# Optimization experiments

Measured on AMD Instinct MI355X. Metric: run time of the kernel, lower is better.

## Reference

```python
import jax, jax.numpy as jnp
import numpy as np

V, E, H, D = 32000, 512, 512, 512  # vocab, emb_dim, enc_hid_dim, dec_hid_dim
B, S, T = 32, 64, 48               # batch, src_len, trg_len


def _gru_cell(x, h, Wih, Whh, bih, bhh):
    # PyTorch GRU cell semantics (gate order r, z, n)
    gi = x @ Wih.T + bih
    gh = h @ Whh.T + bhh
    ir, iz, i_n = jnp.split(gi, 3, axis=-1)
    hr, hz, h_n = jnp.split(gh, 3, axis=-1)
    r = jax.nn.sigmoid(ir + hr)
    z = jax.nn.sigmoid(iz + hz)
    n = jnp.tanh(i_n + r * h_n)
    return (1.0 - z) * n + z * h


def setup_inputs() -> dict:
    key = jax.random.key(0)
    ks = jax.random.split(key, 21)
    f = lambda k, shp: jax.random.normal(k, shp, dtype=jnp.float32) * 0.05
    inp = {
        'src': jax.random.randint(ks[0], (B, S), 0, V),
        'trg': jax.random.randint(ks[1], (T, B), 0, V),
        'emb': f(ks[2], (V, E)),
        'encf_Wih': f(ks[3], (3 * H, E)), 'encf_Whh': f(ks[4], (3 * H, H)),
        'encf_bih': f(ks[5], (3 * H,)), 'encf_bhh': f(ks[6], (3 * H,)),
        'encb_Wih': f(ks[7], (3 * H, E)), 'encb_Whh': f(ks[8], (3 * H, H)),
        'encb_bih': f(ks[9], (3 * H,)), 'encb_bhh': f(ks[10], (3 * H,)),
        'fc_W': f(ks[11], (D, 2 * H)), 'fc_b': f(ks[12], (D,)),
        'attn_W': f(ks[13], (D, D + 2 * H)), 'attn_v': f(ks[14], (D,)),
        'dec_Wih': f(ks[15], (3 * D, E + 2 * H)), 'dec_Whh': f(ks[16], (3 * D, D)),
        'dec_bih': f(ks[17], (3 * D,)), 'dec_bhh': f(ks[18], (3 * D,)),
        'out_W': f(ks[19], (V, 2 * H + D + E)),
        'out_b': jnp.zeros((V,), dtype=jnp.float32),
    }
    return inp


def _forward(src, trg, emb, encf_Wih, encf_Whh, encf_bih, encf_bhh,
             encb_Wih, encb_Whh, encb_bih, encb_bhh, fc_W, fc_b,
             attn_W, attn_v, dec_Wih, dec_Whh, dec_bih, dec_bhh, out_W, out_b):
    x = emb[src]                       # [B,S,E]
    xT = jnp.swapaxes(x, 0, 1)         # [S,B,E]
    h0 = jnp.zeros((src.shape[0], encf_Whh.shape[1]), dtype=x.dtype)

    def stepf(h, xt):
        h2 = _gru_cell(xt, h, encf_Wih, encf_Whh, encf_bih, encf_bhh)
        return h2, h2

    def stepb(h, xt):
        h2 = _gru_cell(xt, h, encb_Wih, encb_Whh, encb_bih, encb_bhh)
        return h2, h2

    hf, yf = jax.lax.scan(stepf, h0, xT)
    hb, yb = jax.lax.scan(stepb, h0, xT[::-1])
    # [B,S,2H] bidirectional encoder outputs (backward stream re-reversed)
    enc_out = jnp.concatenate([jnp.swapaxes(yf, 0, 1), jnp.swapaxes(yb[::-1], 0, 1)], axis=-1)
    # decoder init state from final fwd/bwd hidden
    s0 = jnp.tanh(jnp.concatenate([hf, hb], axis=-1) @ fc_W.T + fc_b)  # [B,D]

    def dec_step(s, tok):
        e = emb[tok]  # [B,E]
        srep = jnp.broadcast_to(s[:, None, :], (s.shape[0], enc_out.shape[1], s.shape[1]))
        energy = jnp.tanh(jnp.concatenate([srep, enc_out], axis=-1) @ attn_W.T)  # [B,S,D]
        a = jax.nn.softmax(energy @ attn_v, axis=1)  # [B,S]
        c = jnp.einsum('bs,bsh->bh', a, enc_out)     # [B,2H]
        s2 = _gru_cell(jnp.concatenate([e, c], axis=-1), s, dec_Wih, dec_Whh, dec_bih, dec_bhh)
        pred = jnp.concatenate([s2, c, e], axis=-1) @ out_W.T + out_b  # [B,V]
        return s2, pred

    # teacher forcing: decoder inputs are trg[0..T-2]
    _, preds = jax.lax.scan(dec_step, s0, trg[:-1])
    out0 = jnp.zeros((1,) + preds.shape[1:], dtype=preds.dtype)  # outputs[0] stays zero
    return jnp.concatenate([out0, preds], axis=0)  # [T,B,V]


def reference(src, trg, emb, encf_Wih, encf_Whh, encf_bih, encf_bhh,
              encb_Wih, encb_Whh, encb_bih, encb_bhh, fc_W, fc_b,
              attn_W, attn_v, dec_Wih, dec_Whh, dec_bih, dec_bhh, out_W, out_b):
    return _forward(src, trg, emb, encf_Wih, encf_Whh, encf_bih, encf_bhh,
                    encb_Wih, encb_Whh, encb_bih, encb_bhh, fc_W, fc_b,
                    attn_W, attn_v, dec_Wih, dec_Whh, dec_bih, dec_bhh, out_W, out_b)
```

## Files before the change

kernel.cpp:

```cpp
#include <hip/hip_runtime.h>
#include <stdint.h>
#include <stddef.h>

typedef __attribute__((ext_vector_type(8))) short short8;
typedef __attribute__((ext_vector_type(4))) float f32x4;
typedef unsigned int u32;

__device__ inline unsigned short f2bf(float f) {
  union { float f; uint32_t u; } v; v.f = f;
  uint32_t u = v.u;
  u += 0x7FFFu + ((u >> 16) & 1u);
  return (unsigned short)(u >> 16);
}
__device__ inline float bf2f(unsigned short h) {
  union { uint32_t u; float f; } v; v.u = ((uint32_t)h) << 16; return v.f;
}
__device__ inline float bflo(u32 v) {
  union { u32 u; float f; } x; x.u = v << 16; return x.f;
}
__device__ inline float bfhi(u32 v) {
  union { u32 u; float f; } x; x.u = v & 0xffff0000u; return x.f;
}
__device__ inline short8 pack8(float4 a, float4 b) {
  short8 r;
  r[0] = (short)f2bf(a.x); r[1] = (short)f2bf(a.y);
  r[2] = (short)f2bf(a.z); r[3] = (short)f2bf(a.w);
  r[4] = (short)f2bf(b.x); r[5] = (short)f2bf(b.y);
  r[6] = (short)f2bf(b.z); r[7] = (short)f2bf(b.w);
  return r;
}
__device__ inline float tanh_fast(float x) {
  float xc = fminf(fmaxf(x, -9.f), 9.f);
  float e = __expf(2.f * xc);
  return (e - 1.f) * __builtin_amdgcn_rcpf(e + 1.f);
}
__device__ inline float sigm_fast(float x) {
  float xc = fminf(fmaxf(x, -30.f), 30.f);
  return __builtin_amdgcn_rcpf(1.f + __expf(-xc));
}
__device__ inline void gl_lds16(const unsigned short* g, unsigned short* l) {
  __builtin_amdgcn_global_load_lds(
      (const __attribute__((address_space(1))) u32*)g,
      (__attribute__((address_space(3))) u32*)l, 16, 0, 0);
}

__global__ __launch_bounds__(128) void prep_gather(
    const int* __restrict__ src, const int* __restrict__ trg,
    const float* __restrict__ emb,
    unsigned short* __restrict__ xbf, unsigned short* __restrict__ ebf,
    unsigned short* __restrict__ Zbf,
    float* __restrict__ outZero,
    unsigned short* __restrict__ hbf,
    float* __restrict__ hf32,
    const float* __restrict__ encfW, const float* __restrict__ encbW,
    const float* __restrict__ attnW, const float* __restrict__ decWhh,
    unsigned short* __restrict__ whFbf, unsigned short* __restrict__ whBbf,
    unsigned short* __restrict__ Wcat) {
  int r = blockIdx.x, tid = threadIdx.x;
  if (r >= 3624) {
    if (tid >= 64) return;
    int q = r - 3624;
    int c = tid * 8;
    const float* s;
    unsigned short* d;
    if (q < 1536) { s = encfW + (size_t)q * 512 + c; d = whFbf + (size_t)q * 512 + c; }
    else if (q < 3072) { int u = q - 1536; s = encbW + (size_t)u * 512 + c; d = whBbf + (size_t)u * 512 + c; }
    else if (q < 3584) { int u = q - 3072; s = attnW + (size_t)u * 1536 + c; d = Wcat + (size_t)u * 512 + c; }
    else { int u = q - 3584; s = decWhh + (size_t)u * 512 + c; d = Wcat + (size_t)(u + 512) * 512 + c; }
    *(short8*)d = pack8(*(const float4*)s, *(const float4*)(s + 4));
    return;
  }
  if (r >= 3584) {
    int z = r - 3584;
    if (z < 32) {
      float4* dst = (float4*)(outZero + (size_t)z * 32000);
      for (int i = tid; i < 8000; i += 128) dst[i] = (float4){0.f, 0.f, 0.f, 0.f};
    } else if (z < 36) {
      float4* dst = (float4*)(hbf + (size_t)(z - 32) * 32768);
      for (int i = tid; i < 4096; i += 128) dst[i] = (float4){0.f, 0.f, 0.f, 0.f};
    } else if (z < 40) {
      float4* dst = (float4*)(hf32 + (size_t)(z - 36) * 32768);
      for (int i = tid; i < 8192; i += 128) dst[i] = (float4){0.f, 0.f, 0.f, 0.f};
    }
    return;
  }
  if (r < 2048) {
    int b = r & 31, s = r >> 5;
    int tok = src[b * 64 + s];
    const float* e = emb + (size_t)tok * 512;
    float4 v = *(const float4*)(e + tid * 4);
    unsigned short* dst = xbf + (size_t)r * 512 + tid * 4;
    dst[0] = f2bf(v.x); dst[1] = f2bf(v.y); dst[2] = f2bf(v.z); dst[3] = f2bf(v.w);
  } else {
    int rr = r - 2048;
    int t = rr >> 5, b = rr & 31;
    unsigned short* dst = ebf + (size_t)rr * 512 + tid * 4;
    if (t < 47) {
      int tok = trg[t * 32 + b];
      const float* e = emb + (size_t)tok * 512;
      float4 v = *(const float4*)(e + tid * 4);
      unsigned short q0 = f2bf(v.x), q1 = f2bf(v.y), q2 = f2bf(v.z), q3 = f2bf(v.w);
      dst[0] = q0; dst[1] = q1; dst[2] = q2; dst[3] = q3;
      unsigned short* zd = Zbf + (size_t)rr * 2048 + 1536 + tid * 4;
      zd[0] = q0; zd[1] = q1; zd[2] = q2; zd[3] = q3;
    } else {
      dst[0] = 0; dst[1] = 0; dst[2] = 0; dst[3] = 0;
    }
  }
}

template <bool ABF, bool BBF, bool WBF>
__device__ inline void gemm_body(
    const void* __restrict__ Av, int lda,
    const void* __restrict__ Bv, int ldb, int bco,
    const float* __restrict__ bias,
    void* __restrict__ Cv, int ldc,
    int K, int Mvalid, int row_off, int m0, int n0) {
  __shared__ __align__(16) unsigned short As[128 * 32];
  __shared__ __align__(16) unsigned short Bs[128 * 32];
  const int tid = threadIdx.x;
  const int w = tid >> 6, lane = tid & 63;
  const int wm = w >> 1, wn = w & 1;
  const int fr = lane & 15, fq = lane >> 4;
  f32x4 acc[4][4];
#pragma unroll
  for (int mi = 0; mi < 4; ++mi)
#pragma unroll
    for (int ni = 0; ni < 4; ++ni) acc[mi][ni] = (f32x4){0.f, 0.f, 0.f, 0.f};
  for (int k0 = 0; k0 < K; k0 += 32) {
#pragma unroll
    for (int p = 0; p < 2; ++p) {
      int idx = p * 256 + tid;
      int row = idx >> 2, seg = idx & 3;
      if (ABF) {
        const unsigned short* Ab = (const unsigned short*)Av;
        *(short8*)(As + row * 32 + seg * 8) =
            *(const short8*)(Ab + (size_t)(m0 + row) * lda + k0 + seg * 8);
      } else {
        const float* Af = (const float*)Av;
        const float* ap = Af + (size_t)(m0 + row) * lda + k0 + seg * 8;
        *(short8*)(As + row * 32 + seg * 8) = pack8(*(const float4*)ap, *(const float4*)(ap + 4));
      }
      if (BBF) {
        const unsigned short* Bb = (const unsigned short*)Bv;
        *(short8*)(Bs + row * 32 + seg * 8) =
            *(const short8*)(Bb + (size_t)(n0 + row) * ldb + bco + k0 + seg * 8);
      } else {
        const float* Bf = (const float*)Bv;
        const float* bp = Bf + (size_t)(n0 + row) * ldb + bco + k0 + seg * 8;
        *(short8*)(Bs + row * 32 + seg * 8) = pack8(*(const float4*)bp, *(const float4*)(bp + 4));
      }
    }
    __syncthreads();
    short8 af[4], bfr[4];
#pragma unroll
    for (int mi = 0; mi < 4; ++mi)
      af[mi] = *(const short8*)(As + (wm * 64 + mi * 16 + fr) * 32 + fq * 8);
#pragma unroll
    for (int ni = 0; ni < 4; ++ni)
      bfr[ni] = *(const short8*)(Bs + (wn * 64 + ni * 16 + fr) * 32 + fq * 8);
#pragma unroll
    for (int mi = 0; mi < 4; ++mi)
#pragma unroll
      for (int ni = 0; ni < 4; ++ni)
        acc[mi][ni] = __builtin_amdgcn_mfma_f32_16x16x32_bf16(af[mi], bfr[ni], acc[mi][ni], 0, 0, 0);
    __syncthreads();
  }
#pragma unroll
  for (int mi = 0; mi < 4; ++mi)
#pragma unroll
    for (int ni = 0; ni < 4; ++ni) {
      int col = n0 + wn * 64 + ni * 16 + fr;
      float bv = bias ? bias[col] : 0.f;
#pragma unroll
      for (int j = 0; j < 4; ++j) {
        int rowm = m0 + wm * 64 + mi * 16 + fq * 4 + j;
        if (rowm < Mvalid) {
          float val = acc[mi][ni][j] + bv;
          if (WBF)
            ((unsigned short*)Cv)[(size_t)(rowm + row_off) * ldc + col] = f2bf(val);
          else
            ((float*)Cv)[(size_t)(rowm + row_off) * ldc + col] = val;
        }
      }
    }
}

template <bool ABF, bool BBF, bool WBF>
__global__ __launch_bounds__(256) void gemm_kernel(
    const void* __restrict__ Av, int lda,
    const void* __restrict__ Bv, int ldb, int bco,
    const float* __restrict__ bias,
    void* __restrict__ Cv, int ldc,
    int K, int Mvalid, int row_off) {
  gemm_body<ABF, BBF, WBF>(Av, lda, Bv, ldb, bco, bias, Cv, ldc, K, Mvalid,
                           row_off, blockIdx.x * 128, blockIdx.y * 128);
}

__global__ __launch_bounds__(256) void gemm_fc(
    const float* __restrict__ hcat, const float* __restrict__ fcW,
    const float* __restrict__ fcb,
    float* __restrict__ sf32, unsigned short* __restrict__ sbf) {
  __shared__ __align__(16) unsigned short As[128 * 32];
  __shared__ __align__(16) unsigned short Bs[128 * 32];
  const int tid = threadIdx.x;
  const int n0 = blockIdx.x * 128;
  const int w = tid >> 6, lane = tid & 63;
  const int wm = w >> 1, wn = w & 1;
  const int fr = lane & 15, fq = lane >> 4;
  f32x4 acc[4][4];
#pragma unroll
  for (int mi = 0; mi < 4; ++mi)
#pragma unroll
    for (int ni = 0; ni < 4; ++ni) acc[mi][ni] = (f32x4){0.f, 0.f, 0.f, 0.f};
  for (int k0 = 0; k0 < 1024; k0 += 32) {
#pragma unroll
    for (int p = 0; p < 2; ++p) {
      int idx = p * 256 + tid;
      int row = idx >> 2, seg = idx & 3;
      if (row < 32) {
        const float* ap = hcat + (size_t)row * 1024 + k0 + seg * 8;
        *(short8*)(As + row * 32 + seg * 8) = pack8(*(const float4*)ap, *(const float4*)(ap + 4));
      }
      const float* bp = fcW + (size_t)(n0 + row) * 1024 + k0 + seg * 8;
      *(short8*)(Bs + row * 32 + seg * 8) = pack8(*(const float4*)bp, *(const float4*)(bp + 4));
    }
    __syncthreads();
    short8 af, bfr[4];
    af = *(const short8*)(As + ((wm == 0 ? fr : fr + 16)) * 32 + fq * 8);
#pragma unroll
    for (int ni = 0; ni < 4; ++ni)
      bfr[ni] = *(const short8*)(Bs + (wn * 64 + ni * 16 + fr) * 32 + fq * 8);
#pragma unroll
    for (int ni = 0; ni < 4; ++ni)
      acc[0][ni] = __builtin_amdgcn_mfma_f32_16x16x32_bf16(af, bfr[ni], acc[0][ni], 0, 0, 0);
    __syncthreads();
  }
#pragma unroll
  for (int ni = 0; ni < 4; ++ni) {
    int col = n0 + wn * 64 + ni * 16 + fr;
    float bv = fcb[col];
#pragma unroll
    for (int j = 0; j < 4; ++j) {
      int rowm = (wm == 0 ? 0 : 16) + fq * 4 + j;
      float val = tanhf(acc[0][ni][j] + bv);
      sf32[(size_t)rowm * 512 + col] = val;
      sbf[(size_t)rowm * 512 + col] = f2bf(val);
    }
  }
}

__global__ __launch_bounds__(256) void gemm_gi(
    const unsigned short* __restrict__ xbf, const unsigned short* __restrict__ ebf,
    const float* __restrict__ encfW, const float* __restrict__ encbW,
    const float* __restrict__ decWih,
    const float* __restrict__ bihF, const float* __restrict__ bihB,
    const float* __restrict__ bihD,
    float* __restrict__ Gif, float* __restrict__ Gib, float* __restrict__ Gie) {
  const int z = blockIdx.z;
  const unsigned short* A;
  const float* B;
  const float* bias;
  float* C;
  int ldb, Mvalid;
  if (z == 0) { A = xbf; B = encfW; ldb = 512; bias = bihF; C = Gif; Mvalid = 2048; }
  else if (z == 1) { A = xbf; B = encbW; ldb = 512; bias = bihB; C = Gib; Mvalid = 2048; }
  else {
    if (blockIdx.x >= 12) return;
    A = ebf; B = decWih; ldb = 1536; bias = bihD; C = Gie; Mvalid = 1536;
  }
  gemm_body<true, false, false>(A, 512, B, ldb, 0, bias, C, 1536, 512, Mvalid, 0,
                                blockIdx.x * 128, blockIdx.y * 128);
}

__global__ __launch_bounds__(256) void gemm_ep(
    const unsigned short* __restrict__ ebo,
    const float* __restrict__ attnW, const float* __restrict__ decWih,
    unsigned short* __restrict__ epf, unsigned short* __restrict__ EP2b) {
  const int z = blockIdx.z;
  if (z == 0 && blockIdx.y >= 4) return;
  if (z == 0)
    gemm_body<true, false, true>(ebo, 1024, attnW, 1536, 512, nullptr, epf, 512,
                                 1024, 2048, 0, blockIdx.x * 128, blockIdx.y * 128);
  else
    gemm_body<true, false, true>(ebo, 1024, decWih, 1536, 512, nullptr, EP2b, 1536,
                                 1024, 2048, 0, blockIdx.x * 128, blockIdx.y * 128);
}

__global__ __launch_bounds__(512, 1) void gemm_big8(
    const unsigned short* __restrict__ A,
    const unsigned short* __restrict__ B,
    const float* __restrict__ bias,
    float* __restrict__ C) {
  extern __shared__ char lds[];
  char* LA = lds;
  char* LB = lds + 65536;
  const int tid = threadIdx.x;
  const int w = tid >> 6, lane = tid & 63;
  int wg = blockIdx.x;
  {
    int x = wg & 7, i = wg >> 3;
    wg = (x < 6 ? x * 94 : 564 + (x - 6) * 93) + i;
  }
  const int m0 = (wg % 6) * 256, n0 = (wg / 6) * 256;
  const int wm = w >> 2, wn = w & 3;
  const int fr = lane & 15, fq = lane >> 4;

  auto stage = [&](const unsigned short* G, char* L, int rowbase, int kt, int h, int c) {
#pragma unroll
    for (int j = 0; j < 2; ++j) {
      int pbh = j * 8192 + w * 1024;
      int pl = pbh + lane * 16;
      int lb = pl ^ (((pl >> 7) & 7) << 4);
      int rl = lb >> 7, ch = (lb >> 4) & 7;
      gl_lds16(G + (size_t)(rowbase + h * 128 + rl) * 2048 + kt * 64 + ch * 8,
               (unsigned short*)(L + c * 32768 + h * 16384 + pbh));
    }
  };

  f32x4 acc[8][4];
#pragma unroll
  for (int mi = 0; mi < 8; ++mi)
#pragma unroll
    for (int ni = 0; ni < 4; ++ni) acc[mi][ni] = (f32x4){0.f, 0.f, 0.f, 0.f};

  stage(A, LA, m0, 0, 0, 0); stage(B, LB, n0, 0, 0, 0);
  stage(A, LA, m0, 0, 1, 0); stage(B, LB, n0, 0, 1, 0);
  asm volatile("s_waitcnt vmcnt(0)" ::: "memory");
  __builtin_amdgcn_s_barrier();

  short8 bfrag[8];
  for (int kt = 0; kt < 32; ++kt) {
    const int c = kt & 1;
    char* Abuf = LA + c * 32768;
    char* Bbuf = LB + c * 32768;
#pragma unroll
    for (int p = 0; p < 4; ++p) {
      if (kt < 31) {
        if (p == 0) {
          stage(A, LA, m0, kt + 1, 0, c ^ 1);
          stage(B, LB, n0, kt + 1, 0, c ^ 1);
        } else if (p == 1) {
          stage(A, LA, m0, kt + 1, 1, c ^ 1);
          stage(B, LB, n0, kt + 1, 1, c ^ 1);
        }
      }
      if (p == 0) {
#pragma unroll
        for (int ni = 0; ni < 4; ++ni)
#pragma unroll
          for (int ks = 0; ks < 2; ++ks) {
            int n = wn * 64 + ni * 16 + fr;
            int h = n >> 7, nl = n & 127;
            int lb = nl * 128 + ks * 64 + fq * 16;
            int pb = lb ^ (((lb >> 7) & 7) << 4);
            bfrag[ni * 2 + ks] = *(const short8*)(Bbuf + h * 16384 + pb);
          }
      }
      short8 afrag[4];
#pragma unroll
      for (int q = 0; q < 2; ++q)
#pragma unroll
        for (int ks = 0; ks < 2; ++ks) {
          int r = wm * 128 + (2 * p + q) * 16 + fr;
          int h = r >> 7, rl = r & 127;
          int lb = rl * 128 + ks * 64 + fq * 16;
          int pb = lb ^ (((lb >> 7) & 7) << 4);
          afrag[q * 2 + ks] = *(const short8*)(Abuf + h * 16384 + pb);
        }
      __builtin_amdgcn_s_setprio(1);
#pragma unroll
      for (int q = 0; q < 2; ++q)
#pragma unroll
        for (int ni = 0; ni < 4; ++ni)
#pragma unroll
          for (int ks = 0; ks < 2; ++ks)
            acc[2 * p + q][ni] = __builtin_amdgcn_mfma_f32_16x16x32_bf16(
                afrag[q * 2 + ks], bfrag[ni * 2 + ks], acc[2 * p + q][ni], 0, 0, 0);
      __builtin_amdgcn_s_setprio(0);
      if (p == 3) asm volatile("s_waitcnt vmcnt(0)" ::: "memory");
      __builtin_amdgcn_s_barrier();
    }
  }
#pragma unroll
  for (int mi = 0; mi < 8; ++mi)
#pragma unroll
    for (int ni = 0; ni < 4; ++ni) {
      int col = n0 + wn * 64 + ni * 16 + fr;
      float bv = bias[col];
#pragma unroll
      for (int j = 0; j < 4; ++j) {
        int row = m0 + wm * 128 + mi * 16 + fq * 4 + j;
        if (row < 1504) C[(size_t)(row + 32) * 32000 + col] = acc[mi][ni][j] + bv;
      }
    }
}

__global__ __launch_bounds__(512) void enc_step(
    const float* __restrict__ Gif, const float* __restrict__ Gib,
    const unsigned short* __restrict__ whFbf, const unsigned short* __restrict__ whBbf,
    const float* __restrict__ bhhF, const float* __restrict__ bhhB,
    unsigned short* __restrict__ hbf,
    float* __restrict__ hf32,
    unsigned short* __restrict__ ebo,
    float* __restrict__ hcat,
    const float* __restrict__ outW, unsigned short* __restrict__ outWbf, int nCvt,
    int t) {
  const int blk = blockIdx.x, tid = threadIdx.x;
  if (blk >= 32) {
    if (blk - 32 < nCvt) {
      size_t base4 = ((size_t)t * nCvt + (blk - 32)) * 1280;
      for (int i = tid; i < 1280; i += 512) {
        float4 v = ((const float4*)outW)[base4 + i];
        unsigned short* d = outWbf + (base4 + i) * 4;
        d[0] = f2bf(v.x); d[1] = f2bf(v.y); d[2] = f2bf(v.z); d[3] = f2bf(v.w);
      }
    }
    return;
  }
  const int dir = blk >> 4, slice = blk & 15, D0 = slice * 32;
  const unsigned short* Wbf = dir ? whBbf : whFbf;
  const float* Gi = dir ? Gib : Gif;
  const float* bhh = dir ? bhhB : bhhF;
  __shared__ __align__(16) unsigned short hlds[32 * 520];
  __shared__ __align__(16) float gl[96 * 33];
  const unsigned short* hb = hbf + dir * 32768 + (t & 1) * 16384;
  for (int c = tid; c < 32 * 64; c += 512) {
    int r = c >> 6, seg = c & 63;
    *(short8*)(hlds + r * 520 + seg * 8) = *(const short8*)(hb + r * 512 + seg * 8);
  }
  __syncthreads();
  const int w = tid >> 6, lane = tid & 63, fr = lane & 15, fq = lane >> 4;
  if (w < 6) {
    int row = w * 16 + fr;
    int gr = (row >> 5) * 512 + D0 + (row & 31);
    const unsigned short* wrow = Wbf + (size_t)gr * 512;
    f32x4 acc0 = {0.f, 0.f, 0.f, 0.f}, acc1 = {0.f, 0.f, 0.f, 0.f};
#pragma unroll
    for (int k0 = 0; k0 < 512; k0 += 32) {
      short8 bq = *(const short8*)(wrow + k0 + fq * 8);
      short8 a0 = *(const short8*)(hlds + fr * 520 + k0 + fq * 8);
      short8 a1 = *(const short8*)(hlds + (16 + fr) * 520 + k0 + fq * 8);
      acc0 = __builtin_amdgcn_mfma_f32_16x16x32_bf16(a0, bq, acc0, 0, 0, 0);
      acc1 = __builtin_amdgcn_mfma_f32_16x16x32_bf16(a1, bq, acc1, 0, 0, 0);
    }
#pragma unroll
    for (int j = 0; j < 4; ++j) {
      gl[row * 33 + fq * 4 + j] = acc0[j];
      gl[row * 33 + 16 + fq * 4 + j] = acc1[j];
    }
  }
  __syncthreads();
  const int srow = dir ? 63 - t : t;
  unsigned short* hnb = hbf + dir * 32768 + ((t + 1) & 1) * 16384;
  const float* hcur = hf32 + dir * 32768 + (t & 1) * 16384;
  float* hnf = hf32 + dir * 32768 + ((t + 1) & 1) * 16384;
#pragma unroll
  for (int rep = 0; rep < 2; ++rep) {
    int idx = rep * 512 + tid, b = idx >> 5, dl = idx & 31, d = D0 + dl;
    float ar = gl[dl * 33 + b] + bhh[d];
    float az = gl[(32 + dl) * 33 + b] + bhh[512 + d];
    float an = gl[(64 + dl) * 33 + b] + bhh[1024 + d];
    const float* gi = Gi + ((size_t)srow * 32 + b) * 1536;
    float r = sigm_fast(gi[d] + ar);
    float z = sigm_fast(gi[512 + d] + az);
    float n = tanh_fast(gi[1024 + d] + r * an);
    float h2 = (1.f - z) * n + z * hcur[b * 512 + d];
    hnb[b * 512 + d] = f2bf(h2);
    hnf[b * 512 + d] = h2;
    ebo[((size_t)b * 64 + srow) * 1024 + (size_t)dir * 512 + d] = f2bf(h2);
    if (t == 63) hcat[(size_t)b * 1024 + (size_t)dir * 512 + d] = h2;
  }
}

__global__ __launch_bounds__(512) void dec_proj(
    const unsigned short* __restrict__ Wcat, const float* __restrict__ decBhh,
    const unsigned short* __restrict__ sbf, float* __restrict__ gout, int t) {
  const int g = blockIdx.x, tid = threadIdx.x;
  __shared__ __align__(16) unsigned short slds[32 * 520];
  const unsigned short* sb = sbf + (t & 1) * 16384;
  for (int c = tid; c < 32 * 64; c += 512) {
    int r = c >> 6, seg = c & 63;
    *(short8*)(slds + r * 520 + seg * 8) = *(const short8*)(sb + r * 512 + seg * 8);
  }
  __syncthreads();
  const int w = tid >> 6, lane = tid & 63, fr = lane & 15, fq = lane >> 4;
  const int mt = w >> 2, nt = w & 3;
  int rc = g * 64 + nt * 16 + fr;
  const unsigned short* wrow = Wcat + (size_t)rc * 512;
  f32x4 acc = {0.f, 0.f, 0.f, 0.f};
#pragma unroll
  for (int k0 = 0; k0 < 512; k0 += 32) {
    short8 a = *(const short8*)(slds + (mt * 16 + fr) * 520 + k0 + fq * 8);
    short8 bq = *(const short8*)(wrow + k0 + fq * 8);
    acc = __builtin_amdgcn_mfma_f32_16x16x32_bf16(a, bq, acc, 0, 0, 0);
  }
  float bv = rc < 512 ? 0.f : decBhh[rc - 512];
#pragma unroll
  for (int j = 0; j < 4; ++j)
    gout[(size_t)(mt * 16 + fq * 4 + j) * 2048 + rc] = acc[j] + bv;
}

__global__ __launch_bounds__(512) void dec_attn(
    const float* __restrict__ attnV,
    const unsigned short* __restrict__ epf,
    const u32* __restrict__ eb32,
    const u32* __restrict__ ep232,
    const float* __restrict__ Gie,
    const float* __restrict__ gout,
    unsigned short* __restrict__ sbf, float* __restrict__ sf32,
    unsigned short* __restrict__ Zbf, int t) {
  const int b = blockIdx.x, tid = threadIdx.x;
  __shared__ __align__(16) float gout_f[2048];
  __shared__ float raw[64], aaw[64];
  __shared__ float vlds[512];
  __shared__ __align__(8) float2 part[5][256];
  vlds[tid] = attnV[tid];
  *(float4*)(gout_f + tid * 4) = *(const float4*)(gout + (size_t)b * 2048 + tid * 4);
  __syncthreads();
  const int s_i = tid >> 3, l8 = tid & 7;
  {
    float part1 = 0.f;
    const float* gp = gout_f + l8 * 64;
    const unsigned short* ep = epf + ((size_t)b * 64 + s_i) * 512 + l8 * 64;
    const float* vv = vlds + l8 * 64;
#pragma unroll
    for (int jc = 0; jc < 8; ++jc) {
      short8 e8 = *(const short8*)(ep + jc * 8);
      float4 g0 = *(const float4*)(gp + jc * 8);
      float4 g1 = *(const float4*)(gp + jc * 8 + 4);
      float4 v0 = *(const float4*)(vv + jc * 8);
      float4 v1 = *(const float4*)(vv + jc * 8 + 4);
      part1 += tanh_fast(g0.x + bf2f((unsigned short)e8[0])) * v0.x;
      part1 += tanh_fast(g0.y + bf2f((unsigned short)e8[1])) * v0.y;
      part1 += tanh_fast(g0.z + bf2f((unsigned short)e8[2])) * v0.z;
      part1 += tanh_fast(g0.w + bf2f((unsigned short)e8[3])) * v0.w;
      part1 += tanh_fast(g1.x + bf2f((unsigned short)e8[4])) * v1.x;
      part1 += tanh_fast(g1.y + bf2f((unsigned short)e8[5])) * v1.y;
      part1 += tanh_fast(g1.z + bf2f((unsigned short)e8[6])) * v1.z;
      part1 += tanh_fast(g1.w + bf2f((unsigned short)e8[7])) * v1.w;
    }
    part1 += __shfl_xor(part1, 1);
    part1 += __shfl_xor(part1, 2);
    part1 += __shfl_xor(part1, 4);
    if (l8 == 0) raw[s_i] = part1;
  }
  __syncthreads();
  if (tid < 64) {
    float x = raw[tid];
    float m = x;
#pragma unroll
    for (int k = 1; k < 64; k <<= 1) m = fmaxf(m, __shfl_xor(m, k));
    float e = __expf(x - m);
    float s = e;
#pragma unroll
    for (int k = 1; k < 64; k <<= 1) s += __shfl_xor(s, k);
    aaw[tid] = e * __builtin_amdgcn_rcpf(s);
  }
  __syncthreads();
  {
    const int cp = tid & 255, sh = tid >> 8;
    const u32* eb = eb32 + (size_t)b * 32768 + cp;
    const u32* e2 = ep232 + (size_t)b * 49152 + cp;
    float p0x = 0.f, p0y = 0.f, p1x = 0.f, p1y = 0.f, p2x = 0.f, p2y = 0.f;
    float p3x = 0.f, p3y = 0.f, p4x = 0.f, p4y = 0.f;
    const int sbase = sh * 32;
#pragma unroll 4
    for (int i = 0; i < 32; ++i) {
      int s2 = sbase + i;
      float a = aaw[s2];
      u32 v0 = eb[(size_t)s2 * 512];
      u32 v1 = eb[(size_t)s2 * 512 + 256];
      u32 v2 = e2[(size_t)s2 * 768];
      u32 v3 = e2[(size_t)s2 * 768 + 256];
      u32 v4 = e2[(size_t)s2 * 768 + 512];
      p0x += a * bflo(v0); p0y += a * bfhi(v0);
      p1x += a * bflo(v1); p1y += a * bfhi(v1);
      p2x += a * bflo(v2); p2y += a * bfhi(v2);
      p3x += a * bflo(v3); p3y += a * bfhi(v3);
      p4x += a * bflo(v4); p4y += a * bfhi(v4);
    }
    if (sh == 0) {
      part[0][cp] = make_float2(p0x, p0y);
      part[1][cp] = make_float2(p1x, p1y);
      part[2][cp] = make_float2(p2x, p2y);
      part[3][cp] = make_float2(p3x, p3y);
      part[4][cp] = make_float2(p4x, p4y);
    }
    __syncthreads();
    if (sh == 1) {
      part[0][cp].x += p0x; part[0][cp].y += p0y;
      part[1][cp].x += p1x; part[1][cp].y += p1y;
      part[2][cp].x += p2x; part[2][cp].y += p2y;
      part[3][cp].x += p3x; part[3][cp].y += p3y;
      part[4][cp].x += p4x; part[4][cp].y += p4y;
    }
  }
  __syncthreads();
  size_t zrow = ((size_t)t * 32 + b) * 2048;
  {
    int slot = tid >> 8, cp2 = tid & 255;
    float2 cpair = part[slot][cp2];
    u32 pk = (u32)f2bf(cpair.x) | ((u32)f2bf(cpair.y) << 16);
    *(u32*)(Zbf + zrow + 512 + (size_t)(slot * 256 + cp2) * 2) = pk;
  }
  {
    int hp = tid >> 1, odd = tid & 1;
    float g0a = odd ? part[2][hp].y : part[2][hp].x;
    float g1a = odd ? part[3][hp].y : part[3][hp].x;
    float g2a = odd ? part[4][hp].y : part[4][hp].x;
    const float* gie = Gie + ((size_t)t * 32 + b) * 1536;
    float sprev = sf32[(t & 1) * 16384 + b * 512 + tid];
    float rr = sigm_fast(gie[tid] + g0a + gout_f[512 + tid]);
    float zz = sigm_fast(gie[512 + tid] + g1a + gout_f[1024 + tid]);
    float nn = tanh_fast(gie[1024 + tid] + g2a + rr * gout_f[1536 + tid]);
    float s2v = (1.f - zz) * nn + zz * sprev;
    sbf[((t + 1) & 1) * 16384 + b * 512 + tid] = f2bf(s2v);
    sf32[((t + 1) & 1) * 16384 + b * 512 + tid] = s2v;
    Zbf[zrow + tid] = f2bf(s2v);
  }
}

extern "C" void kernel_launch(void* const* d_in, const int* in_sizes, int n_in,
                              void* d_out, int out_size, void* d_ws, size_t ws_size,
                              hipStream_t stream) {
  (void)in_sizes; (void)n_in; (void)out_size;
  const int* src = (const int*)d_in[0];
  const int* trg = (const int*)d_in[1];
  const float* emb = (const float*)d_in[2];
  const float* encf_Wih = (const float*)d_in[3];
  const float* encf_Whh = (const float*)d_in[4];
  const float* encf_bih = (const float*)d_in[5];
  const float* encf_bhh = (const float*)d_in[6];
  const float* encb_Wih = (const float*)d_in[7];
  const float* encb_Whh = (const float*)d_in[8];
  const float* encb_bih = (const float*)d_in[9];
  const float* encb_bhh = (const float*)d_in[10];
  const float* fc_W = (const float*)d_in[11];
  const float* fc_b = (const float*)d_in[12];
  const float* attn_W = (const float*)d_in[13];
  const float* attn_v = (const float*)d_in[14];
  const float* dec_Wih = (const float*)d_in[15];
  const float* dec_Whh = (const float*)d_in[16];
  const float* dec_bih = (const float*)d_in[17];
  const float* dec_bhh = (const float*)d_in[18];
  const float* out_W = (const float*)d_in[19];
  const float* out_b = (const float*)d_in[20];
  float* out = (float*)d_out;

  char* p = (char*)d_ws;
  size_t off = 0;
  auto alloc = [&](size_t bytes) {
    void* r = p + off;
    off = (off + bytes + 255) & ~(size_t)255;
    return r;
  };
  unsigned short* xbf = (unsigned short*)alloc((size_t)2048 * 512 * 2);
  unsigned short* ebf = (unsigned short*)alloc((size_t)1536 * 512 * 2);
  unsigned short* Zbf = (unsigned short*)alloc((size_t)1536 * 2048 * 2);
  float* Gif = (float*)alloc((size_t)2048 * 1536 * 4);
  float* Gib = (float*)alloc((size_t)2048 * 1536 * 4);
  float* Gie = (float*)alloc((size_t)1536 * 1536 * 4);
  unsigned short* ebo = (unsigned short*)alloc((size_t)2048 * 1024 * 2);
  unsigned short* epf = (unsigned short*)alloc((size_t)2048 * 512 * 2);
  unsigned short* EP2b = (unsigned short*)alloc((size_t)2048 * 1536 * 2);
  unsigned short* whFbf = (unsigned short*)alloc((size_t)1536 * 512 * 2);
  unsigned short* whBbf = (unsigned short*)alloc((size_t)1536 * 512 * 2);
  unsigned short* Wcat = (unsigned short*)alloc((size_t)2048 * 512 * 2);
  unsigned short* hbf = (unsigned short*)alloc((size_t)2 * 2 * 32 * 512 * 2);
  float* hf32 = (float*)alloc((size_t)2 * 2 * 32 * 512 * 4);
  float* hcat = (float*)alloc((size_t)32 * 1024 * 4);
  unsigned short* sbf = (unsigned short*)alloc((size_t)2 * 32 * 512 * 2);
  float* sf32 = (float*)alloc((size_t)2 * 32 * 512 * 4);
  float* gout = (float*)alloc((size_t)32 * 2048 * 4);
  unsigned short* outWbf = (unsigned short*)alloc((size_t)32000 * 2048 * 2);
  const bool bigB = (off <= ws_size);

  prep_gather<<<8744, 128, 0, stream>>>(src, trg, emb, xbf, ebf, Zbf,
                                        out, hbf, hf32,
                                        encf_Whh, encb_Whh, attn_W, dec_Whh,
                                        whFbf, whBbf, Wcat);

  gemm_gi<<<dim3(16, 12, 3), 256, 0, stream>>>(
      xbf, ebf, encf_Wih, encb_Wih, dec_Wih, encf_bih, encb_bih, dec_bih,
      Gif, Gib, Gie);

  const int nCvt = bigB ? 200 : 0;
  for (int t = 0; t < 64; ++t)
    enc_step<<<32 + nCvt, 512, 0, stream>>>(Gif, Gib, whFbf, whBbf, encf_bhh, encb_bhh,
                                            hbf, hf32, ebo, hcat, out_W, outWbf, nCvt, t);

  gemm_fc<<<4, 256, 0, stream>>>(hcat, fc_W, fc_b, sf32, sbf);

  gemm_ep<<<dim3(16, 12, 2), 256, 0, stream>>>(ebo, attn_W, dec_Wih, epf, EP2b);

  for (int t = 0; t < 47; ++t) {
    dec_proj<<<32, 512, 0, stream>>>(Wcat, dec_bhh, sbf, gout, t);
    dec_attn<<<32, 512, 0, stream>>>(attn_v, epf, (const u32*)ebo, (const u32*)EP2b,
                                     Gie, gout, sbf, sf32, Zbf, t);
  }

  if (bigB) {
    hipFuncSetAttribute((const void*)gemm_big8,
                        hipFuncAttributeMaxDynamicSharedMemorySize, 131072);
    gemm_big8<<<750, 512, 131072, stream>>>(Zbf, outWbf, out_b, out);
  } else {
    gemm_kernel<true, false, false><<<dim3(12, 250), 256, 0, stream>>>(
        Zbf, 2048, out_W, 2048, 0, out_b, out, 32000, 2048, 1504, 32);
  }
}
```

Measured before the change: 1.616 ms.

## Switch output GEMM to triple-buffered K=32 pipeline with new LDS swizzle

```diff
diff --git a/kernel.cpp b/kernel.cpp
--- a/kernel.cpp
+++ b/kernel.cpp
@@ -293,8 +293,6 @@
     const float* __restrict__ bias,
     float* __restrict__ C) {
   extern __shared__ char lds[];
-  char* LA = lds;
-  char* LB = lds + 65536;
   const int tid = threadIdx.x;
   const int w = tid >> 6, lane = tid & 63;
   int wg = blockIdx.x;
@@ -305,18 +303,24 @@
   const int m0 = (wg % 6) * 256, n0 = (wg / 6) * 256;
   const int wm = w >> 2, wn = w & 3;
   const int fr = lane & 15, fq = lane >> 4;
-
-  auto stage = [&](const unsigned short* G, char* L, int rowbase, int kt, int h, int c) {
+  const int srow = lane >> 2;
+  const int sch = (((lane & 3) ^ (srow & 3)) * 8);
+
+  auto stage = [&](int kt, int c) {
+    char* LA = lds + c * 32768;
+    char* LB = LA + 16384;
 #pragma unroll
     for (int j = 0; j < 2; ++j) {
-      int pbh = j * 8192 + w * 1024;
-      int pl = pbh + lane * 16;
-      int lb = pl ^ (((pl >> 7) & 7) << 4);
-      int rl = lb >> 7, ch = (lb >> 4) & 7;
-      gl_lds16(G + (size_t)(rowbase + h * 128 + rl) * 2048 + kt * 64 + ch * 8,
-               (unsigned short*)(L + c * 32768 + h * 16384 + pbh));
+      int rb = w * 32 + j * 16;
+      int rg = rb + srow;
+      int ch = (((lane & 3) ^ ((rg ^ (rg >> 2)) & 3)) * 8);
+      gl_lds16(A + (size_t)(m0 + rg) * 2048 + kt * 32 + ch,
+               (unsigned short*)(LA + rb * 64));
+      gl_lds16(B + (size_t)(n0 + rg) * 2048 + kt * 32 + ch,
+               (unsigned short*)(LB + rb * 64));
     }
   };
+  (void)sch;
 
   f32x4 acc[8][4];
 #pragma unroll
@@ -324,63 +328,40 @@
 #pragma unroll
     for (int ni = 0; ni < 4; ++ni) acc[mi][ni] = (f32x4){0.f, 0.f, 0.f, 0.f};
 
-  stage(A, LA, m0, 0, 0, 0); stage(B, LB, n0, 0, 0, 0);
-  stage(A, LA, m0, 0, 1, 0); stage(B, LB, n0, 0, 1, 0);
-  asm volatile("s_waitcnt vmcnt(0)" ::: "memory");
-  __builtin_amdgcn_s_barrier();
-
-  short8 bfrag[8];
-  for (int kt = 0; kt < 32; ++kt) {
-    const int c = kt & 1;
-    char* Abuf = LA + c * 32768;
-    char* Bbuf = LB + c * 32768;
-#pragma unroll
-    for (int p = 0; p < 4; ++p) {
-      if (kt < 31) {
-        if (p == 0) {
-          stage(A, LA, m0, kt + 1, 0, c ^ 1);
-          stage(B, LB, n0, kt + 1, 0, c ^ 1);
-        } else if (p == 1) {
-          stage(A, LA, m0, kt + 1, 1, c ^ 1);
-          stage(B, LB, n0, kt + 1, 1, c ^ 1);
-        }
-      }
-      if (p == 0) {
-#pragma unroll
-        for (int ni = 0; ni < 4; ++ni)
-#pragma unroll
-          for (int ks = 0; ks < 2; ++ks) {
-            int n = wn * 64 + ni * 16 + fr;
-            int h = n >> 7, nl = n & 127;
-            int lb = nl * 128 + ks * 64 + fq * 16;
-            int pb = lb ^ (((lb >> 7) & 7) << 4);
-            bfrag[ni * 2 + ks] = *(const short8*)(Bbuf + h * 16384 + pb);
-          }
-      }
-      short8 afrag[4];
-#pragma unroll
-      for (int q = 0; q < 2; ++q)
-#pragma unroll
-        for (int ks = 0; ks < 2; ++ks) {
-          int r = wm * 128 + (2 * p + q) * 16 + fr;
-          int h = r >> 7, rl = r & 127;
-          int lb = rl * 128 + ks * 64 + fq * 16;
-          int pb = lb ^ (((lb >> 7) & 7) << 4);
-          afrag[q * 2 + ks] = *(const short8*)(Abuf + h * 16384 + pb);
-        }
-      __builtin_amdgcn_s_setprio(1);
-#pragma unroll
-      for (int q = 0; q < 2; ++q)
-#pragma unroll
-        for (int ni = 0; ni < 4; ++ni)
-#pragma unroll
-          for (int ks = 0; ks < 2; ++ks)
-            acc[2 * p + q][ni] = __builtin_amdgcn_mfma_f32_16x16x32_bf16(
-                afrag[q * 2 + ks], bfrag[ni * 2 + ks], acc[2 * p + q][ni], 0, 0, 0);
-      __builtin_amdgcn_s_setprio(0);
-      if (p == 3) asm volatile("s_waitcnt vmcnt(0)" ::: "memory");
-      __builtin_amdgcn_s_barrier();
-    }
+  stage(0, 0);
+  stage(1, 1);
+
+  int c = 0, cn = 2;
+  for (int kt = 0; kt < 64; ++kt) {
+    if (kt < 63) asm volatile("s_waitcnt vmcnt(4)" ::: "memory");
+    else asm volatile("s_waitcnt vmcnt(0)" ::: "memory");
+    __builtin_amdgcn_s_barrier();
+    char* LA = lds + c * 32768;
+    char* LB = LA + 16384;
+    short8 bfrag[4], afrag[8];
+#pragma unroll
+    for (int ni = 0; ni < 4; ++ni) {
+      int r = wn * 64 + ni * 16 + fr;
+      int pb = r * 64 + ((fq * 16) ^ ((((r ^ (r >> 2)) & 3)) << 4));
+      bfrag[ni] = *(const short8*)(LB + pb);
+    }
+#pragma unroll
+    for (int mi = 0; mi < 8; ++mi) {
+      int r = wm * 128 + mi * 16 + fr;
+      int pb = r * 64 + ((fq * 16) ^ ((((r ^ (r >> 2)) & 3)) << 4));
+      afrag[mi] = *(const short8*)(LA + pb);
+    }
+    __builtin_amdgcn_s_setprio(1);
+#pragma unroll
+    for (int mi = 0; mi < 8; ++mi)
+#pragma unroll
+      for (int ni = 0; ni < 4; ++ni)
+        acc[mi][ni] = __builtin_amdgcn_mfma_f32_16x16x32_bf16(
+            afrag[mi], bfrag[ni], acc[mi][ni], 0, 0, 0);
+    __builtin_amdgcn_s_setprio(0);
+    if (kt < 62) stage(kt + 2, cn);
+    c = (c == 2) ? 0 : c + 1;
+    cn = (cn == 2) ? 0 : cn + 1;
   }
 #pragma unroll
   for (int mi = 0; mi < 8; ++mi)
@@ -702,8 +683,8 @@
 
   if (bigB) {
     hipFuncSetAttribute((const void*)gemm_big8,
-                        hipFuncAttributeMaxDynamicSharedMemorySize, 131072);
-    gemm_big8<<<750, 512, 131072, stream>>>(Zbf, outWbf, out_b, out);
+                        hipFuncAttributeMaxDynamicSharedMemorySize, 98304);
+    gemm_big8<<<750, 512, 98304, stream>>>(Zbf, outWbf, out_b, out);
   } else {
     gemm_kernel<true, false, false><<<dim3(12, 250), 256, 0, stream>>>(
         Zbf, 2048, out_W, 2048, 0, out_b, out, 32000, 2048, 1504, 32);
```

Result: no change. 1.639 ms (+1.4%).
